# Performance work log

Hardware: AMD Instinct MI355X
Metric: run time of the kernel (lower is better)

The kernel has to match this reference:

```python
import jax, jax.numpy as jnp
import numpy as np

N_NODES = 50000
N_EDGES = 600000
IN_DIM = 128
HID = 128
N_CLASSES = 40
N_GRAPHS = 128


def setup_inputs() -> dict:
    key = jax.random.key(0)
    ks = jax.random.split(key, 12)
    x = jax.random.normal(ks[0], (N_NODES, IN_DIM), dtype=jnp.float32)
    edge_index = jax.random.randint(ks[1], (2, N_EDGES), 0, N_NODES, dtype=jnp.int64)
    batch = jnp.sort(jax.random.randint(ks[2], (N_NODES,), 0, N_GRAPHS, dtype=jnp.int64))
    dims = [IN_DIM, HID, HID, N_CLASSES]
    params = {}
    for l in range(3):
        d_in, d_out = dims[l], dims[l + 1]
        s = 1.0 / np.sqrt(d_in)
        params[f"Wl{l}"] = jax.random.uniform(ks[3 + 3 * l], (d_out, d_in), jnp.float32, -s, s)
        params[f"bl{l}"] = jax.random.uniform(ks[4 + 3 * l], (d_out,), jnp.float32, -s, s)
        params[f"Wr{l}"] = jax.random.uniform(ks[5 + 3 * l], (d_out, d_in), jnp.float32, -s, s)
    return {"x": x, "edge_index": edge_index, "batch": batch, **params}


def _sage_layer(h, src, dst, Wl, bl, Wr):
    # message: relu(x_j) (edge_attr is None -> zero), mean-aggregate at dst
    m = jnp.maximum(h[src], 0.0)                       # [E, d]
    agg = jax.ops.segment_sum(m, dst, num_segments=N_NODES)
    cnt = jax.ops.segment_sum(jnp.ones((m.shape[0],), h.dtype), dst, num_segments=N_NODES)
    agg = agg / jnp.maximum(cnt, 1.0)[:, None]
    # lin_l(agg) + lin_r(x)
    return agg @ Wl.T + bl + h @ Wr.T


def reference(x, edge_index, batch, Wl0, bl0, Wr0, Wl1, bl1, Wr1, Wl2, bl2, Wr2):
    src, dst = edge_index[0], edge_index[1]
    Ws = [(Wl0, bl0, Wr0), (Wl1, bl1, Wr1), (Wl2, bl2, Wr2)]
    h = x
    for l, (Wl, bl, Wr) in enumerate(Ws):
        # dropout is identity in eval mode
        h = _sage_layer(h, src, dst, Wl, bl, Wr)
        if l != len(Ws) - 1:
            h = jnp.maximum(h, 0.0)
    # global mean pool over graphs
    gsum = jax.ops.segment_sum(h, batch, num_segments=N_GRAPHS)
    gcnt = jax.ops.segment_sum(jnp.ones((h.shape[0],), h.dtype), batch, num_segments=N_GRAPHS)
    g = gsum / jnp.maximum(gcnt, 1.0)[:, None]
    return h, g
```

## Files before the change

kernel.cpp:

```cpp
#include <hip/hip_runtime.h>
#include <hip/hip_bf16.h>


#define NODES 50000
#define K_DIM 128
#define N_GRAPHS 128

typedef __attribute__((ext_vector_type(8))) short short8;
typedef __attribute__((ext_vector_type(4))) short short4v;
typedef __attribute__((ext_vector_type(4))) float f32x4;

__device__ inline short f2bf(float f) {
    unsigned u = __builtin_bit_cast(unsigned, f);
    u += 0x7FFFu + ((u >> 16) & 1u);
    return (short)(u >> 16);
}
__device__ inline float bf2f(short h) {
    unsigned u = ((unsigned)(unsigned short)h) << 16;
    return __builtin_bit_cast(float, u);
}
__device__ inline float blo(unsigned u) { return __builtin_bit_cast(float, u << 16); }
__device__ inline float bhi(unsigned u) { return __builtin_bit_cast(float, u & 0xFFFF0000u); }
__device__ inline unsigned hilo_pack(float f) {
    short h = f2bf(f);
    short l = f2bf(f - bf2f(h));
    return ((unsigned)(unsigned short)h) | (((unsigned)(unsigned short)l) << 16);
}

__global__ void init_kernel(const float* __restrict__ w0, const float* __restrict__ w1,
                            const float* __restrict__ w2, const float* __restrict__ w3,
                            const float* __restrict__ w4, const float* __restrict__ w5,
                            short* __restrict__ whi, short* __restrict__ wlo,
                            int* __restrict__ deg, const int* __restrict__ batch,
                            int* __restrict__ gstart, int* __restrict__ counter,
                            const float* __restrict__ x, short* __restrict__ xb,
                            float* __restrict__ gsum, int N) {
    int idx = blockIdx.x * 256 + threadIdx.x;
    if (idx < N * (K_DIM / 4)) {
        float4 v = reinterpret_cast<const float4*>(x)[idx];
        short4v b;
        b[0] = f2bf(fmaxf(v.x, 0.f));
        b[1] = f2bf(fmaxf(v.y, 0.f));
        b[2] = f2bf(fmaxf(v.z, 0.f));
        b[3] = f2bf(fmaxf(v.w, 0.f));
        *reinterpret_cast<short4v*>(&xb[idx * 4]) = b;
    }
    if (idx < N) deg[idx] = 0;
    if (idx < N_GRAPHS * 40) gsum[idx] = 0.f;
    if (idx == 0) *counter = 0;
    const int TOT = 4 * 16384 + 96 * 128;
    if (idx < TOT) {
        float v;
        if (idx < 65536) {
            int m = idx >> 14, i2 = idx & 16383;
            const float* W = (m == 0) ? w0 : (m == 1) ? w1 : (m == 2) ? w2 : w3;
            int t1 = i2 >> 9, rem = i2 & 511;
            int lane = rem >> 3, e = rem & 7;
            int wv_ = t1 >> 3, nt = (t1 >> 2) & 1, kc = t1 & 3;
            int quad = lane >> 4, l15 = lane & 15;
            int n = wv_ * 32 + nt * 16 + l15;
            int k = kc * 32 + quad * 8 + e;
            v = W[n * 128 + k];
        } else {
            int i2 = idx - 65536;
            int t2 = i2 >> 9, rem = i2 & 511;
            int lane = rem >> 3, e = rem & 7;
            int nt2 = t2 >> 2, kc = t2 & 3;
            int quad = lane >> 4, l15 = lane & 15;
            int n = nt2 * 16 + l15;
            int k = kc * 32 + quad * 8 + e;
            if (t2 < 20) {
                v = (n < 40) ? w4[n * 128 + k] : w5[(n - 40) * 128 + k];
            } else {
                v = 0.f;
            }
        }
        unsigned p = hilo_pack(v);
        whi[idx] = (short)(p & 0xFFFFu);
        wlo[idx] = (short)(p >> 16);
    }
    if (idx <= N_GRAPHS) {
        int g = idx;
        int lo = 0, hi = N;
        while (lo < hi) {
            int mid = (lo + hi) >> 1;
            if (batch[mid] < g) lo = mid + 1; else hi = mid;
        }
        gstart[g] = lo;
    }
}

__global__ void deg_kernel(const int* __restrict__ dst, int* __restrict__ deg, int E) {
    int e = blockIdx.x * blockDim.x + threadIdx.x;
    if (e < E) atomicAdd(&deg[dst[e]], 1);
}

__global__ void csr_offsets(const int* __restrict__ deg, int* __restrict__ counter,
                            int* __restrict__ rowptr, int* __restrict__ fillpos, int N) {
    const int tid = threadIdx.x, lane = tid & 63, wv = tid >> 6;
    int i = blockIdx.x * 256 + tid;
    int v = (i < N) ? deg[i] : 0;
    int incl = v;
    #pragma unroll
    for (int off = 1; off < 64; off <<= 1) {
        int t = __shfl_up(incl, off, 64);
        if (lane >= off) incl += t;
    }
    __shared__ int ws[4];
    __shared__ int sbase;
    if (lane == 63) ws[wv] = incl;
    __syncthreads();
    if (tid == 0) sbase = atomicAdd(counter, ws[0] + ws[1] + ws[2] + ws[3]);
    __syncthreads();
    int add = sbase;
    for (int k = 0; k < wv; ++k) add += ws[k];
    int excl = add + incl - v;
    if (i < N) { rowptr[i] = excl; fillpos[i] = excl; }
}

__global__ void fill_kernel(const int* __restrict__ src, const int* __restrict__ dst,
                            int* __restrict__ fillpos, int* __restrict__ csr_src, int E) {
    int e = blockIdx.x * blockDim.x + threadIdx.x;
    if (e < E) {
        int p = atomicAdd(&fillpos[dst[e]], 1);
        csr_src[p] = src[e];
    }
}

__global__ void agg_bf16(const unsigned short* __restrict__ hb,
                         const int* __restrict__ rowptr, const int* __restrict__ deg,
                         const int* __restrict__ csr_src,
                         short* __restrict__ aggb, int N) {
    int w = (blockIdx.x * blockDim.x + threadIdx.x) >> 6;
    if (w >= N) return;
    int lane = threadIdx.x & 63;
    int slot = lane >> 4, l16 = lane & 15;
    int s = rowptr[w];
    int e = s + deg[w];
    const uint4* T = reinterpret_cast<const uint4*>(hb);
    float2 a0 = make_float2(0.f, 0.f), a1 = a0, a2 = a0, a3 = a0;
    int i = s + slot;
    for (; i + 4 < e; i += 8) {
        uint4 va = T[(size_t)csr_src[i] * 16 + l16];
        uint4 vb = T[(size_t)csr_src[i + 4] * 16 + l16];
        a0.x += blo(va.x) + blo(vb.x); a0.y += bhi(va.x) + bhi(vb.x);
        a1.x += blo(va.y) + blo(vb.y); a1.y += bhi(va.y) + bhi(vb.y);
        a2.x += blo(va.z) + blo(vb.z); a2.y += bhi(va.z) + bhi(vb.z);
        a3.x += blo(va.w) + blo(vb.w); a3.y += bhi(va.w) + bhi(vb.w);
    }
    for (; i < e; i += 4) {
        uint4 va = T[(size_t)csr_src[i] * 16 + l16];
        a0.x += blo(va.x); a0.y += bhi(va.x);
        a1.x += blo(va.y); a1.y += bhi(va.y);
        a2.x += blo(va.z); a2.y += bhi(va.z);
        a3.x += blo(va.w); a3.y += bhi(va.w);
    }
    #pragma unroll
    for (int off = 16; off <= 32; off <<= 1) {
        a0.x += __shfl_xor(a0.x, off, 64); a0.y += __shfl_xor(a0.y, off, 64);
        a1.x += __shfl_xor(a1.x, off, 64); a1.y += __shfl_xor(a1.y, off, 64);
        a2.x += __shfl_xor(a2.x, off, 64); a2.y += __shfl_xor(a2.y, off, 64);
        a3.x += __shfl_xor(a3.x, off, 64); a3.y += __shfl_xor(a3.y, off, 64);
    }
    if (slot == 0) {
        float inv = 1.0f / fmaxf((float)(e - s), 1.0f);
        short8 b;
        b[0] = f2bf(a0.x * inv); b[1] = f2bf(a0.y * inv);
        b[2] = f2bf(a1.x * inv); b[3] = f2bf(a1.y * inv);
        b[4] = f2bf(a2.x * inv); b[5] = f2bf(a2.y * inv);
        b[6] = f2bf(a3.x * inv); b[7] = f2bf(a3.y * inv);
        *reinterpret_cast<short8*>(&aggb[(size_t)w * K_DIM + l16 * 8]) = b;
    }
}

__global__ __launch_bounds__(256) void sage0_mfma(
        const short* __restrict__ Ab_in, const float* __restrict__ Xf,
        const short* __restrict__ Bhl, const short* __restrict__ Bll,
        const short* __restrict__ Bhr, const short* __restrict__ Blr,
        const float* __restrict__ bl,
        short* __restrict__ outHi, short* __restrict__ outLo, int N) {
    constexpr int BM = 64;
    constexpr int LSTR = 40;
    const int tid = threadIdx.x;
    const int lane = tid & 63;
    const int wave = tid >> 6;
    const int l15 = lane & 15;
    const int quad = lane >> 4;
    const int m0 = blockIdx.x * BM;
    const int srow = tid >> 2, sc8 = tid & 3;

    __shared__ __align__(16) short Ab [BM * LSTR];
    __shared__ __align__(16) short Ahi[BM * LSTR];
    __shared__ __align__(16) short Alo[BM * LSTR];

    f32x4 acc[4][2];
    #pragma unroll
    for (int i = 0; i < 4; ++i)
        #pragma unroll
        for (int j = 0; j < 2; ++j) acc[i][j] = (f32x4){0.f, 0.f, 0.f, 0.f};

    const short8 zero8 = (short8){0, 0, 0, 0, 0, 0, 0, 0};
    const int sm = m0 + srow;

    for (int k0 = 0; k0 < K_DIM; k0 += 32) {
        const int kc = k0 >> 5;
        __syncthreads();
        {
            short8 va = zero8, vh = zero8, vl = zero8;
            if (sm < N) {
                va = *reinterpret_cast<const short8*>(Ab_in + (size_t)sm * K_DIM + k0 + sc8 * 8);
                const float* xp = Xf + (size_t)sm * K_DIM + k0 + sc8 * 8;
                float4 f0 = *reinterpret_cast<const float4*>(xp);
                float4 f1 = *reinterpret_cast<const float4*>(xp + 4);
                float fv[8] = {f0.x, f0.y, f0.z, f0.w, f1.x, f1.y, f1.z, f1.w};
                #pragma unroll
                for (int j = 0; j < 8; ++j) {
                    unsigned p = hilo_pack(fv[j]);
                    vh[j] = (short)(p & 0xFFFFu);
                    vl[j] = (short)(p >> 16);
                }
            }
            *reinterpret_cast<short8*>(&Ab [srow * LSTR + sc8 * 8]) = va;
            *reinterpret_cast<short8*>(&Ahi[srow * LSTR + sc8 * 8]) = vh;
            *reinterpret_cast<short8*>(&Alo[srow * LSTR + sc8 * 8]) = vl;
        }
        short8 bhl_[2], bll_[2], bhr_[2], blr_[2];
        #pragma unroll
        for (int nt = 0; nt < 2; ++nt) {
            size_t base = ((size_t)(((wave * 2 + nt) * 4 + kc) * 64 + lane)) * 8;
            bhl_[nt] = *reinterpret_cast<const short8*>(Bhl + base);
            bll_[nt] = *reinterpret_cast<const short8*>(Bll + base);
            bhr_[nt] = *reinterpret_cast<const short8*>(Bhr + base);
            blr_[nt] = *reinterpret_cast<const short8*>(Blr + base);
        }
        __syncthreads();
        #pragma unroll
        for (int mt = 0; mt < 4; ++mt) {
            int row = mt * 16 + l15;
            short8 ab = *reinterpret_cast<const short8*>(&Ab [row * LSTR + quad * 8]);
            short8 ah = *reinterpret_cast<const short8*>(&Ahi[row * LSTR + quad * 8]);
            short8 ao = *reinterpret_cast<const short8*>(&Alo[row * LSTR + quad * 8]);
            #pragma unroll
            for (int nt = 0; nt < 2; ++nt) {
                acc[mt][nt] = __builtin_amdgcn_mfma_f32_16x16x32_bf16(ab, bhl_[nt], acc[mt][nt], 0, 0, 0);
                acc[mt][nt] = __builtin_amdgcn_mfma_f32_16x16x32_bf16(ab, bll_[nt], acc[mt][nt], 0, 0, 0);
                acc[mt][nt] = __builtin_amdgcn_mfma_f32_16x16x32_bf16(ah, bhr_[nt], acc[mt][nt], 0, 0, 0);
                acc[mt][nt] = __builtin_amdgcn_mfma_f32_16x16x32_bf16(ah, blr_[nt], acc[mt][nt], 0, 0, 0);
                acc[mt][nt] = __builtin_amdgcn_mfma_f32_16x16x32_bf16(ao, bhr_[nt], acc[mt][nt], 0, 0, 0);
            }
        }
    }

    #pragma unroll
    for (int mt = 0; mt < 4; ++mt) {
        #pragma unroll
        for (int nt = 0; nt < 2; ++nt) {
            int col = wave * 32 + nt * 16 + l15;
            float b = bl[col];
            #pragma unroll
            for (int reg = 0; reg < 4; ++reg) {
                int row = m0 + mt * 16 + quad * 4 + reg;
                if (row < N) {
                    float v = fmaxf(acc[mt][nt][reg] + b, 0.f);
                    unsigned p = hilo_pack(v);
                    outHi[(size_t)row * K_DIM + col] = (short)(p & 0xFFFFu);
                    outLo[(size_t)row * K_DIM + col] = (short)(p >> 16);
                }
            }
        }
    }
}

__global__ __launch_bounds__(256) void sage1_gemm80(
        const short* __restrict__ Ab_in,
        const short* __restrict__ Hhi_in, const short* __restrict__ Hlo_in,
        const short* __restrict__ Bhl, const short* __restrict__ Bll,
        const short* __restrict__ Bhr, const short* __restrict__ Blr,
        const float* __restrict__ bl,
        const short* __restrict__ B2h, const short* __restrict__ B2l,
        const float* __restrict__ b2,
        short* __restrict__ ylb, float* __restrict__ yr40, int N) {
    constexpr int BM = 32;
    constexpr int LSTA = 136;
    const int tid = threadIdx.x;
    const int lane = tid & 63;
    const int wave = tid >> 6;
    const int l15 = lane & 15;
    const int quad = lane >> 4;
    const int m0 = blockIdx.x * BM;

    __shared__ __align__(16) short SH[3 * BM * LSTA];
    short* AbL = SH;
    short* AhL = SH + BM * LSTA;
    short* AlL = SH + 2 * BM * LSTA;
    short* H2h = SH;
    short* H2l = SH + BM * LSTA;

    f32x4 acc[2][2];
    #pragma unroll
    for (int i = 0; i < 2; ++i)
        #pragma unroll
        for (int j = 0; j < 2; ++j) acc[i][j] = (f32x4){0.f, 0.f, 0.f, 0.f};

    const short8 zero8 = (short8){0, 0, 0, 0, 0, 0, 0, 0};

    {
        const int srow = tid >> 3;
        const int c0 = (tid & 7) * 16;
        const int sm = m0 + srow;
        short8 a0 = zero8, a1 = zero8, h0 = zero8, h1 = zero8, l0 = zero8, l1 = zero8;
        if (sm < N) {
            const short* pa = Ab_in  + (size_t)sm * K_DIM + c0;
            const short* ph = Hhi_in + (size_t)sm * K_DIM + c0;
            const short* pl = Hlo_in + (size_t)sm * K_DIM + c0;
            a0 = *reinterpret_cast<const short8*>(pa);
            a1 = *reinterpret_cast<const short8*>(pa + 8);
            h0 = *reinterpret_cast<const short8*>(ph);
            h1 = *reinterpret_cast<const short8*>(ph + 8);
            l0 = *reinterpret_cast<const short8*>(pl);
            l1 = *reinterpret_cast<const short8*>(pl + 8);
        }
        *reinterpret_cast<short8*>(&AbL[srow * LSTA + c0])     = a0;
        *reinterpret_cast<short8*>(&AbL[srow * LSTA + c0 + 8]) = a1;
        *reinterpret_cast<short8*>(&AhL[srow * LSTA + c0])     = h0;
        *reinterpret_cast<short8*>(&AhL[srow * LSTA + c0 + 8]) = h1;
        *reinterpret_cast<short8*>(&AlL[srow * LSTA + c0])     = l0;
        *reinterpret_cast<short8*>(&AlL[srow * LSTA + c0 + 8]) = l1;
    }
    __syncthreads();

    #pragma unroll
    for (int kc = 0; kc < 4; ++kc) {
        const int k0 = kc * 32;
        short8 bhl_[2], bll_[2], bhr_[2], blr_[2];
        #pragma unroll
        for (int nt = 0; nt < 2; ++nt) {
            size_t base = ((size_t)(((wave * 2 + nt) * 4 + kc) * 64 + lane)) * 8;
            bhl_[nt] = *reinterpret_cast<const short8*>(Bhl + base);
            bll_[nt] = *reinterpret_cast<const short8*>(Bll + base);
            bhr_[nt] = *reinterpret_cast<const short8*>(Bhr + base);
            blr_[nt] = *reinterpret_cast<const short8*>(Blr + base);
        }
        #pragma unroll
        for (int mt = 0; mt < 2; ++mt) {
            int row = mt * 16 + l15;
            short8 ab = *reinterpret_cast<const short8*>(&AbL[row * LSTA + k0 + quad * 8]);
            short8 ah = *reinterpret_cast<const short8*>(&AhL[row * LSTA + k0 + quad * 8]);
            short8 ao = *reinterpret_cast<const short8*>(&AlL[row * LSTA + k0 + quad * 8]);
            #pragma unroll
            for (int nt = 0; nt < 2; ++nt) {
                acc[mt][nt] = __builtin_amdgcn_mfma_f32_16x16x32_bf16(ab, bhl_[nt], acc[mt][nt], 0, 0, 0);
                acc[mt][nt] = __builtin_amdgcn_mfma_f32_16x16x32_bf16(ab, bll_[nt], acc[mt][nt], 0, 0, 0);
                acc[mt][nt] = __builtin_amdgcn_mfma_f32_16x16x32_bf16(ah, bhr_[nt], acc[mt][nt], 0, 0, 0);
                acc[mt][nt] = __builtin_amdgcn_mfma_f32_16x16x32_bf16(ah, blr_[nt], acc[mt][nt], 0, 0, 0);
                acc[mt][nt] = __builtin_amdgcn_mfma_f32_16x16x32_bf16(ao, bhr_[nt], acc[mt][nt], 0, 0, 0);
            }
        }
    }

    __syncthreads();

    #pragma unroll
    for (int mt = 0; mt < 2; ++mt) {
        #pragma unroll
        for (int nt = 0; nt < 2; ++nt) {
            int col = wave * 32 + nt * 16 + l15;
            float b = bl[col];
            #pragma unroll
            for (int reg = 0; reg < 4; ++reg) {
                int row = mt * 16 + quad * 4 + reg;
                float v = fmaxf(acc[mt][nt][reg] + b, 0.f);
                unsigned p = hilo_pack(v);
                H2h[row * LSTA + col] = (short)(p & 0xFFFFu);
                H2l[row * LSTA + col] = (short)(p >> 16);
            }
        }
    }
    __syncthreads();

    const int rg = wave >> 1, ch = wave & 1;
    const int NT = ch ? 2 : 3;
    const int ntb = ch ? 3 : 0;
    f32x4 c2[3];
    #pragma unroll
    for (int j = 0; j < 3; ++j) c2[j] = (f32x4){0.f, 0.f, 0.f, 0.f};
    const int arow = rg * 16 + l15;

    #pragma unroll
    for (int kc = 0; kc < 4; ++kc) {
        const int k0 = kc * 32;
        short8 ah = *reinterpret_cast<const short8*>(&H2h[arow * LSTA + k0 + quad * 8]);
        short8 ao = *reinterpret_cast<const short8*>(&H2l[arow * LSTA + k0 + quad * 8]);
        for (int j = 0; j < NT; ++j) {
            size_t base = ((size_t)(((ntb + j) * 4 + kc) * 64 + lane)) * 8;
            short8 bh = *reinterpret_cast<const short8*>(B2h + base);
            short8 bo = *reinterpret_cast<const short8*>(B2l + base);
            c2[j] = __builtin_amdgcn_mfma_f32_16x16x32_bf16(ah, bh, c2[j], 0, 0, 0);
            c2[j] = __builtin_amdgcn_mfma_f32_16x16x32_bf16(ah, bo, c2[j], 0, 0, 0);
            c2[j] = __builtin_amdgcn_mfma_f32_16x16x32_bf16(ao, bh, c2[j], 0, 0, 0);
        }
    }

    for (int j = 0; j < NT; ++j) {
        int col = (ntb + j) * 16 + l15;
        #pragma unroll
        for (int reg = 0; reg < 4; ++reg) {
            int row = m0 + rg * 16 + quad * 4 + reg;
            if (row < N) {
                float v = c2[j][reg];
                if (col < 40) {
                    ylb[(size_t)row * 40 + col] = f2bf(v);
                } else {
                    yr40[(size_t)row * 40 + (col - 40)] = v + b2[col - 40];
                }
            }
        }
    }
}

__global__ __launch_bounds__(256) void agg40_pool(
        const unsigned int* __restrict__ ylbu, const float* __restrict__ yr40,
        const int* __restrict__ rowptr, const int* __restrict__ deg,
        const int* __restrict__ csr_src,
        const int* __restrict__ batch, const int* __restrict__ gstart,
        float* __restrict__ out, float* __restrict__ gsum, int N) {
    const int w = (blockIdx.x * blockDim.x + threadIdx.x) >> 6;
    const int lane = threadIdx.x & 63;
    const int wv = threadIdx.x >> 6;
    const int half = lane >> 5, l32 = lane & 31;
    __shared__ float sh[4][40];
    __shared__ int sg[4];
    __shared__ float sinv[4];

    if (w < N) {
        int s = rowptr[w], e = s + deg[w];
        float ax = 0.f, ay = 0.f;
        if (l32 < 20) {
            int i = s + half;
            for (; i + 6 < e; i += 8) {
                int s0 = csr_src[i], s1 = csr_src[i + 2], s2 = csr_src[i + 4], s3 = csr_src[i + 6];
                unsigned v0 = ylbu[(size_t)s0 * 20 + l32];
                unsigned v1 = ylbu[(size_t)s1 * 20 + l32];
                unsigned v2 = ylbu[(size_t)s2 * 20 + l32];
                unsigned v3 = ylbu[(size_t)s3 * 20 + l32];
                ax += (blo(v0) + blo(v1)) + (blo(v2) + blo(v3));
                ay += (bhi(v0) + bhi(v1)) + (bhi(v2) + bhi(v3));
            }
            for (; i < e; i += 2) {
                unsigned v0 = ylbu[(size_t)csr_src[i] * 20 + l32];
                ax += blo(v0); ay += bhi(v0);
            }
        }
        ax += __shfl_xor(ax, 32, 64);
        ay += __shfl_xor(ay, 32, 64);
        if (half == 0 && l32 < 20) {
            float inv = 1.0f / fmaxf((float)(e - s), 1.0f);
            float2 yr = *reinterpret_cast<const float2*>(&yr40[(size_t)w * 40 + 2 * l32]);
            float vx = ax * inv + yr.x;
            float vy = ay * inv + yr.y;
            *reinterpret_cast<float2*>(&out[(size_t)w * 40 + 2 * l32]) = make_float2(vx, vy);
            sh[wv][2 * l32]     = vx;
            sh[wv][2 * l32 + 1] = vy;
        }
    }
    if (lane == 0) {
        if (w < N) {
            int g = batch[w];
            sg[wv] = g;
            sinv[wv] = 1.0f / fmaxf((float)(gstart[g + 1] - gstart[g]), 1.0f);
        } else {
            sg[wv] = -1;
        }
    }
    __syncthreads();
    if (wv == 0 && lane < 40) {
        int cur = -1;
        float accum = 0.f;
        #pragma unroll
        for (int k = 0; k < 4; ++k) {
            int gk = sg[k];
            if (gk < 0) continue;
            float c = sh[k][lane] * sinv[k];
            if (gk == cur) {
                accum += c;
            } else {
                if (cur >= 0) atomicAdd(&gsum[cur * 40 + lane], accum);
                cur = gk;
                accum = c;
            }
        }
        if (cur >= 0) atomicAdd(&gsum[cur * 40 + lane], accum);
    }
}

extern "C" void kernel_launch(void* const* d_in, const int* in_sizes, int n_in,
                              void* d_out, int out_size, void* d_ws, size_t ws_size,
                              hipStream_t stream) {
    const float* x    = (const float*)d_in[0];
    const int*   ei   = (const int*)d_in[1];
    const int*   batch= (const int*)d_in[2];
    const float* Wl0  = (const float*)d_in[3];
    const float* bl0  = (const float*)d_in[4];
    const float* Wr0  = (const float*)d_in[5];
    const float* Wl1  = (const float*)d_in[6];
    const float* bl1  = (const float*)d_in[7];
    const float* Wr1  = (const float*)d_in[8];
    const float* Wl2  = (const float*)d_in[9];
    const float* bl2  = (const float*)d_in[10];
    const float* Wr2  = (const float*)d_in[11];

    const int N = in_sizes[0] / K_DIM;
    const int E = in_sizes[1] / 2;
    const int* src = ei;
    const int* dst = ei + E;

    float* out = (float*)d_out;
    float* gsum = out + (size_t)N * 40;

    char* w = (char*)d_ws;
    auto alloc = [&](size_t bytes) {
        char* p = w;
        w += (bytes + 255) & ~(size_t)255;
        return p;
    };
    const size_t PL = (size_t)N * K_DIM * 2;
    short* aggb  = (short*)alloc(PL);
    short* xb    = (short*)alloc(PL);
    short* h1hi  = (short*)alloc(PL);
    short* h1lo  = (short*)alloc(PL);
    short* ylb   = (short*)alloc((size_t)N * 40 * 2);
    float* yr40  = (float*)alloc((size_t)N * 40 * 4);
    int*   rowptr= (int*)alloc((size_t)(N + 1) * 4);
    int*   deg   = (int*)alloc((size_t)N * 4);
    int*   fillp = (int*)alloc((size_t)N * 4);
    int*   csr   = (int*)alloc((size_t)E * 4);
    int*   counter = (int*)alloc(256);
    int*   gstart= (int*)alloc((size_t)(N_GRAPHS + 1) * 4);
    short* whi   = (short*)alloc(77824 * 2);
    short* wlo   = (short*)alloc(77824 * 2);

    const int NB = (N + 255) / 256;
    const int initGrid = (N * (K_DIM / 4) + 255) / 256;

    init_kernel<<<initGrid, 256, 0, stream>>>(Wl0, Wr0, Wl1, Wr1, Wl2, Wr2,
                                              whi, wlo, deg, batch, gstart, counter,
                                              x, xb, gsum, N);
    deg_kernel<<<(E + 255) / 256, 256, 0, stream>>>(dst, deg, E);
    csr_offsets<<<NB, 256, 0, stream>>>(deg, counter, rowptr, fillp, N);
    fill_kernel<<<(E + 255) / 256, 256, 0, stream>>>(src, dst, fillp, csr, E);

    short* hWl0 = whi;          short* lWl0 = wlo;
    short* hWr0 = whi + 16384;  short* lWr0 = wlo + 16384;
    short* hWl1 = whi + 32768;  short* lWl1 = wlo + 32768;
    short* hWr1 = whi + 49152;  short* lWr1 = wlo + 49152;
    short* hW2  = whi + 65536;  short* lW2  = wlo + 65536;

    const int aggGrid   = (N * 64 + 255) / 256;
    const int gemmGrid  = (N + 63) / 64;
    const int gemmGrid32= (N + 31) / 32;

    agg_bf16<<<aggGrid, 256, 0, stream>>>((const unsigned short*)xb, rowptr, deg, csr, aggb, N);
    sage0_mfma<<<gemmGrid, 256, 0, stream>>>(
        aggb, x, hWl0, lWl0, hWr0, lWr0, bl0, h1hi, h1lo, N);
    agg_bf16<<<aggGrid, 256, 0, stream>>>((const unsigned short*)h1hi, rowptr, deg, csr, aggb, N);
    sage1_gemm80<<<gemmGrid32, 256, 0, stream>>>(
        aggb, h1hi, h1lo, hWl1, lWl1, hWr1, lWr1, bl1, hW2, lW2, bl2, ylb, yr40, N);
    agg40_pool<<<aggGrid, 256, 0, stream>>>((const unsigned int*)ylb, yr40,
                                            rowptr, deg, csr, batch, gstart, out, gsum, N);
}
```

Measured before the change: 292.1 us.

## Load full-K A tile once in sage0 GEMM with 32-row blocks

The layer-0 GEMM now uses 32-row tiles and stages the entire 128-wide K slice of the aggregated, hi and lo A operands into shared memory in one pass. This replaces four K-chunk iterations that each had two barriers with a single barrier. The grid doubles to 1563 blocks for better occupancy and latency hiding. The cost is that B fragments are reloaded from global memory by twice as many blocks, and each block uses more shared memory.

```diff
diff --git a/kernel.cpp b/kernel.cpp
--- a/kernel.cpp
+++ b/kernel.cpp
@@ -179,51 +179,69 @@
         const short* __restrict__ Bhr, const short* __restrict__ Blr,
         const float* __restrict__ bl,
         short* __restrict__ outHi, short* __restrict__ outLo, int N) {
-    constexpr int BM = 64;
-    constexpr int LSTR = 40;
+    constexpr int BM = 32;
+    constexpr int LSTA = 136;
     const int tid = threadIdx.x;
     const int lane = tid & 63;
     const int wave = tid >> 6;
     const int l15 = lane & 15;
     const int quad = lane >> 4;
     const int m0 = blockIdx.x * BM;
-    const int srow = tid >> 2, sc8 = tid & 3;
-
-    __shared__ __align__(16) short Ab [BM * LSTR];
-    __shared__ __align__(16) short Ahi[BM * LSTR];
-    __shared__ __align__(16) short Alo[BM * LSTR];
-
-    f32x4 acc[4][2];
-    #pragma unroll
-    for (int i = 0; i < 4; ++i)
+
+    __shared__ __align__(16) short SH[3 * BM * LSTA];
+    short* AbL = SH;
+    short* AhL = SH + BM * LSTA;
+    short* AlL = SH + 2 * BM * LSTA;
+
+    f32x4 acc[2][2];
+    #pragma unroll
+    for (int i = 0; i < 2; ++i)
         #pragma unroll
         for (int j = 0; j < 2; ++j) acc[i][j] = (f32x4){0.f, 0.f, 0.f, 0.f};
 
     const short8 zero8 = (short8){0, 0, 0, 0, 0, 0, 0, 0};
-    const int sm = m0 + srow;
-
-    for (int k0 = 0; k0 < K_DIM; k0 += 32) {
-        const int kc = k0 >> 5;
-        __syncthreads();
-        {
-            short8 va = zero8, vh = zero8, vl = zero8;
-            if (sm < N) {
-                va = *reinterpret_cast<const short8*>(Ab_in + (size_t)sm * K_DIM + k0 + sc8 * 8);
-                const float* xp = Xf + (size_t)sm * K_DIM + k0 + sc8 * 8;
-                float4 f0 = *reinterpret_cast<const float4*>(xp);
-                float4 f1 = *reinterpret_cast<const float4*>(xp + 4);
-                float fv[8] = {f0.x, f0.y, f0.z, f0.w, f1.x, f1.y, f1.z, f1.w};
-                #pragma unroll
-                for (int j = 0; j < 8; ++j) {
-                    unsigned p = hilo_pack(fv[j]);
-                    vh[j] = (short)(p & 0xFFFFu);
-                    vl[j] = (short)(p >> 16);
-                }
-            }
-            *reinterpret_cast<short8*>(&Ab [srow * LSTR + sc8 * 8]) = va;
-            *reinterpret_cast<short8*>(&Ahi[srow * LSTR + sc8 * 8]) = vh;
-            *reinterpret_cast<short8*>(&Alo[srow * LSTR + sc8 * 8]) = vl;
-        }
+
+    {
+        const int srow = tid >> 3;
+        const int c0 = (tid & 7) * 16;
+        const int sm = m0 + srow;
+        short8 a0 = zero8, a1 = zero8, h0 = zero8, h1 = zero8, l0 = zero8, l1 = zero8;
+        if (sm < N) {
+            const short* pa = Ab_in + (size_t)sm * K_DIM + c0;
+            a0 = *reinterpret_cast<const short8*>(pa);
+            a1 = *reinterpret_cast<const short8*>(pa + 8);
+            const float* xp = Xf + (size_t)sm * K_DIM + c0;
+            float4 f0 = *reinterpret_cast<const float4*>(xp);
+            float4 f1 = *reinterpret_cast<const float4*>(xp + 4);
+            float4 f2 = *reinterpret_cast<const float4*>(xp + 8);
+            float4 f3 = *reinterpret_cast<const float4*>(xp + 12);
+            float fv[16] = {f0.x, f0.y, f0.z, f0.w, f1.x, f1.y, f1.z, f1.w,
+                            f2.x, f2.y, f2.z, f2.w, f3.x, f3.y, f3.z, f3.w};
+            #pragma unroll
+            for (int j = 0; j < 8; ++j) {
+                unsigned p = hilo_pack(fv[j]);
+                h0[j] = (short)(p & 0xFFFFu);
+                l0[j] = (short)(p >> 16);
+            }
+            #pragma unroll
+            for (int j = 0; j < 8; ++j) {
+                unsigned p = hilo_pack(fv[8 + j]);
+                h1[j] = (short)(p & 0xFFFFu);
+                l1[j] = (short)(p >> 16);
+            }
+        }
+        *reinterpret_cast<short8*>(&AbL[srow * LSTA + c0])     = a0;
+        *reinterpret_cast<short8*>(&AbL[srow * LSTA + c0 + 8]) = a1;
+        *reinterpret_cast<short8*>(&AhL[srow * LSTA + c0])     = h0;
+        *reinterpret_cast<short8*>(&AhL[srow * LSTA + c0 + 8]) = h1;
+        *reinterpret_cast<short8*>(&AlL[srow * LSTA + c0])     = l0;
+        *reinterpret_cast<short8*>(&AlL[srow * LSTA + c0 + 8]) = l1;
+    }
+    __syncthreads();
+
+    #pragma unroll
+    for (int kc = 0; kc < 4; ++kc) {
+        const int k0 = kc * 32;
         short8 bhl_[2], bll_[2], bhr_[2], blr_[2];
         #pragma unroll
         for (int nt = 0; nt < 2; ++nt) {
@@ -233,13 +251,12 @@
             bhr_[nt] = *reinterpret_cast<const short8*>(Bhr + base);
             blr_[nt] = *reinterpret_cast<const short8*>(Blr + base);
         }
-        __syncthreads();
-        #pragma unroll
-        for (int mt = 0; mt < 4; ++mt) {
+        #pragma unroll
+        for (int mt = 0; mt < 2; ++mt) {
             int row = mt * 16 + l15;
-            short8 ab = *reinterpret_cast<const short8*>(&Ab [row * LSTR + quad * 8]);
-            short8 ah = *reinterpret_cast<const short8*>(&Ahi[row * LSTR + quad * 8]);
-            short8 ao = *reinterpret_cast<const short8*>(&Alo[row * LSTR + quad * 8]);
+            short8 ab = *reinterpret_cast<const short8*>(&AbL[row * LSTA + k0 + quad * 8]);
+            short8 ah = *reinterpret_cast<const short8*>(&AhL[row * LSTA + k0 + quad * 8]);
+            short8 ao = *reinterpret_cast<const short8*>(&AlL[row * LSTA + k0 + quad * 8]);
             #pragma unroll
             for (int nt = 0; nt < 2; ++nt) {
                 acc[mt][nt] = __builtin_amdgcn_mfma_f32_16x16x32_bf16(ab, bhl_[nt], acc[mt][nt], 0, 0, 0);
@@ -252,7 +269,7 @@
     }
 
     #pragma unroll
-    for (int mt = 0; mt < 4; ++mt) {
+    for (int mt = 0; mt < 2; ++mt) {
         #pragma unroll
         for (int nt = 0; nt < 2; ++nt) {
             int col = wave * 32 + nt * 16 + l15;
@@ -556,11 +573,10 @@
     short* hW2  = whi + 65536;  short* lW2  = wlo + 65536;
 
     const int aggGrid   = (N * 64 + 255) / 256;
-    const int gemmGrid  = (N + 63) / 64;
     const int gemmGrid32= (N + 31) / 32;
 
     agg_bf16<<<aggGrid, 256, 0, stream>>>((const unsigned short*)xb, rowptr, deg, csr, aggb, N);
-    sage0_mfma<<<gemmGrid, 256, 0, stream>>>(
+    sage0_mfma<<<gemmGrid32, 256, 0, stream>>>(
         aggb, x, hWl0, lWl0, hWr0, lWr0, bl0, h1hi, h1lo, N);
     agg_bf16<<<aggGrid, 256, 0, stream>>>((const unsigned short*)h1hi, rowptr, deg, csr, aggb, N);
     sage1_gemm80<<<gemmGrid32, 256, 0, stream>>>(
```

Result: no change. 294.4 us (+0.8%).
